# Kernel tuning notes

Measured on AMD Instinct MI355X. Metric: run time of the kernel, lower is better.

Reference implementation:

```python
import jax, jax.numpy as jnp
import numpy as np

D_MODEL = 1024
NHEAD = 16
D_K = 64
D_V = 64
B, S = 4, 2048
LN_EPS = 1e-5


def setup_inputs() -> dict:
    key = jax.random.key(0)
    ks = jax.random.split(key, 8)
    inv = 1.0 / np.sqrt(D_MODEL)
    return {
        "Q_input": jax.random.normal(ks[0], (B, S, D_MODEL), jnp.float32),
        "K_input": jax.random.normal(ks[1], (B, S, D_MODEL), jnp.float32),
        "V_input": jax.random.normal(ks[2], (B, S, D_MODEL), jnp.float32),
        "attn_mask": jnp.zeros((B, S, S), dtype=bool),
        # Linear weights stored as [in, out] for x @ W
        "W_Q": jax.random.uniform(ks[3], (D_MODEL, NHEAD * D_K), jnp.float32, -inv, inv),
        "W_K": jax.random.uniform(ks[4], (D_MODEL, NHEAD * D_K), jnp.float32, -inv, inv),
        "W_V": jax.random.uniform(ks[5], (D_MODEL, NHEAD * D_V), jnp.float32, -inv, inv),
        "W_fc": jax.random.uniform(ks[6], (NHEAD * D_V, D_MODEL), jnp.float32, -inv, inv),
        "ln_gamma": jnp.ones((D_MODEL,), jnp.float32),
        "ln_beta": jnp.zeros((D_MODEL,), jnp.float32),
    }


def reference(Q_input, K_input, V_input, attn_mask, W_Q, W_K, W_V, W_fc, ln_gamma, ln_beta):
    b = Q_input.shape[0]
    # QKV projections -> [b, h, s, d]
    Q = (Q_input @ W_Q).reshape(b, -1, NHEAD, D_K).transpose(0, 2, 1, 3)
    K = (K_input @ W_K).reshape(b, -1, NHEAD, D_K).transpose(0, 2, 1, 3)
    V = (V_input @ W_V).reshape(b, -1, NHEAD, D_V).transpose(0, 2, 1, 3)
    # NOTE faithful quirk: divide by sqrt(temperature) = sqrt(sqrt(d_k)) = d_k**0.25
    scale = np.sqrt(D_K ** 0.5).astype(np.float32)
    score = jnp.einsum('bhqd,bhkd->bhqk', Q, K) / scale
    score = jnp.where(attn_mask[:, None, :, :], jnp.float32(-1e9), score)
    attn = jax.nn.softmax(score, axis=-1)
    out = jnp.einsum('bhqk,bhkd->bhqd', attn, V)  # [b,h,s,d_v]
    out = out.transpose(0, 2, 1, 3).reshape(b, -1, NHEAD * D_V)
    q = out @ W_fc + Q_input  # residual
    mu = jnp.mean(q, axis=-1, keepdims=True)
    var = jnp.mean(jnp.square(q - mu), axis=-1, keepdims=True)
    q = (q - mu) / jnp.sqrt(var + LN_EPS) * ln_gamma + ln_beta
    return (q, attn)
```

## Files before the change

### kernel.cpp

```cpp
#include <hip/hip_runtime.h>
#include <hip/hip_bf16.h>
#include <stdint.h>

#define D_MODEL 1024
#define NHEAD   16
#define DK      64
#define BB      4
#define SS      2048
#define MROWS   (BB*SS)
#define KDIM    1024

typedef __attribute__((ext_vector_type(8))) short short8;
typedef __attribute__((ext_vector_type(4))) short bf16x4;
typedef __attribute__((ext_vector_type(4))) float f32x4;

static __device__ __forceinline__ unsigned short f2bf(float f) {
    union { float f; unsigned u; } v; v.f = f;
    unsigned r = v.u + 0x7FFFu + ((v.u >> 16) & 1u);
    return (unsigned short)(r >> 16);
}
static __device__ __forceinline__ float bf2f(unsigned short s) {
    union { unsigned u; float f; } v; v.u = ((unsigned)s) << 16;
    return v.f;
}

#define LDS_RD8(base, byteoff) (*(const short8*)((const char*)(base) + (byteoff)))

__global__ __launch_bounds__(256) void k_conv(const float* __restrict__ src,
                                              unsigned short* __restrict__ dst, int n) {
    int i = (blockIdx.x * 256 + threadIdx.x) * 4;
    if (i < n) {
        float4 v = *(const float4*)(src + i);
        ushort4 o;
        o.x = f2bf(v.x); o.y = f2bf(v.y); o.z = f2bf(v.z); o.w = f2bf(v.w);
        *(ushort4*)(dst + i) = o;
    }
}

__global__ __launch_bounds__(256) void k_transpose(const float* __restrict__ W,
                                                   unsigned short* __restrict__ WT) {
    __shared__ float t[32][33];
    int bx = blockIdx.x, by = blockIdx.y;
    int tx = threadIdx.x & 31, ty = threadIdx.x >> 5;
#pragma unroll
    for (int k = 0; k < 4; k++) {
        int r = by * 32 + ty + k * 8;
        t[ty + k * 8][tx] = W[(size_t)r * 1024 + bx * 32 + tx];
    }
    __syncthreads();
#pragma unroll
    for (int k = 0; k < 4; k++) {
        int c = bx * 32 + ty + k * 8;
        WT[(size_t)c * 1024 + by * 32 + tx] = f2bf(t[tx][ty + k * 8]);
    }
}

template<int MODE>
__global__ __launch_bounds__(256) void k_gemm(const unsigned short* __restrict__ A,
                                              const unsigned short* __restrict__ BT,
                                              unsigned short* __restrict__ out,
                                              const float* __restrict__ resid) {
    __shared__ __align__(16) unsigned short As[128 * 32];
    __shared__ __align__(16) unsigned short Bs[128 * 32];
    int m0 = blockIdx.x * 128;
    int n0 = blockIdx.y * 128;
    int tid = threadIdx.x;
    int lane = tid & 63, w = tid >> 6;
    int wm = w >> 1, wn = w & 1;
    int lo = lane & 15, hi = lane >> 4;

    f32x4 acc[4][4];
#pragma unroll
    for (int i = 0; i < 4; i++)
#pragma unroll
        for (int j = 0; j < 4; j++) acc[i][j] = (f32x4){0.f, 0.f, 0.f, 0.f};

    for (int k0 = 0; k0 < KDIM; k0 += 32) {
#pragma unroll
        for (int c = 0; c < 2; c++) {
            int idx = c * 256 + tid;
            int row = idx >> 2, ko = (idx & 3) * 8;
            __builtin_amdgcn_global_load_lds(
                (const __attribute__((address_space(1))) void*)(A + (size_t)(m0 + row) * KDIM + k0 + ko),
                (__attribute__((address_space(3))) void*)((char*)As + idx * 16), 16, 0, 0);
            __builtin_amdgcn_global_load_lds(
                (const __attribute__((address_space(1))) void*)(BT + (size_t)(n0 + row) * KDIM + k0 + ko),
                (__attribute__((address_space(3))) void*)((char*)Bs + idx * 16), 16, 0, 0);
        }
        __syncthreads();
        short8 a[4], b[4];
#pragma unroll
        for (int i = 0; i < 4; i++)
            a[i] = *(const short8*)(As + (wm * 64 + i * 16 + lo) * 32 + hi * 8);
#pragma unroll
        for (int j = 0; j < 4; j++)
            b[j] = *(const short8*)(Bs + (wn * 64 + j * 16 + lo) * 32 + hi * 8);
#pragma unroll
        for (int i = 0; i < 4; i++)
#pragma unroll
            for (int j = 0; j < 4; j++)
                acc[i][j] = __builtin_amdgcn_mfma_f32_16x16x32_bf16(a[i], b[j], acc[i][j], 0, 0, 0);
        __syncthreads();
    }

#pragma unroll
    for (int i = 0; i < 4; i++)
#pragma unroll
        for (int j = 0; j < 4; j++)
#pragma unroll
            for (int r = 0; r < 4; r++) {
                int m = m0 + wm * 64 + i * 16 + hi * 4 + r;
                int n = n0 + wn * 64 + j * 16 + lo;
                float v = acc[i][j][r];
                if (MODE == 0 || MODE == 3) {
                    if (MODE == 3) v *= 0.35355339059327373f;
                    int b_ = m >> 11, s = m & 2047, h = n >> 6, d = n & 63;
                    out[(((size_t)(b_ * NHEAD + h)) * SS + s) * DK + d] = f2bf(v);
                } else if (MODE == 1) {
                    int b_ = m >> 11, s = m & 2047, h = n >> 6, d = n & 63;
                    out[(((size_t)(b_ * NHEAD + h)) * DK + d) * SS + s] = f2bf(v);
                } else {
                    v += resid[(size_t)m * D_MODEL + n];
                    out[(size_t)m * D_MODEL + n] = f2bf(v);
                }
            }
}

static __device__ __forceinline__ void stage64(const unsigned short* __restrict__ src_base,
                                               size_t row_stride_elts,
                                               unsigned short* lds, int tid) {
#pragma unroll
    for (int i = 0; i < 2; i++) {
        int idx = i * 256 + tid;
        int r = idx >> 3, c = idx & 7;
        int sc = c ^ (r & 7);
        __builtin_amdgcn_global_load_lds(
            (const __attribute__((address_space(1))) void*)(src_base + (size_t)r * row_stride_elts + sc * 8),
            (__attribute__((address_space(3))) void*)(lds + idx * 8), 16, 0, 0);
    }
}

__global__ __launch_bounds__(256) void k_attn(const unsigned short* __restrict__ Qb,
                                              const unsigned short* __restrict__ Kb,
                                              const unsigned short* __restrict__ VTb,
                                              float* __restrict__ attn_out,
                                              unsigned short* __restrict__ O) {
    __shared__ __align__(16) unsigned short Kl[2][64 * 64];
    __shared__ __align__(16) unsigned short Vl[2][64 * 64];
    __shared__ __align__(16) unsigned short Pl[4][16 * 64];

    int bid = blockIdx.x;
    int bh = (bid & 7) * 8 + ((bid >> 3) & 7);
    int qt = bid >> 6;

    int tid = threadIdx.x;
    int w = tid >> 6, lane = tid & 63;
    int lo = lane & 15, hi = lane >> 4;
    int lo7 = lo & 7;

    const unsigned short* Qh = Qb + (size_t)bh * SS * DK;
    const unsigned short* Kh = Kb + (size_t)bh * SS * DK;
    const unsigned short* Vh = VTb + (size_t)bh * DK * SS;
    int q0 = qt * 64 + w * 16;

    short8 qa0 = *(const short8*)(Qh + (size_t)(q0 + lo) * DK + hi * 8);
    short8 qa1 = *(const short8*)(Qh + (size_t)(q0 + lo) * DK + 32 + hi * 8);

    float lsum = 0.f;
    stage64(Kh, DK, Kl[0], tid);
    {
        int cur = 0;
        for (int kt = 0; kt < SS; kt += 64, cur ^= 1) {
            __syncthreads();
            if (kt + 64 < SS) stage64(Kh + (size_t)(kt + 64) * DK, DK, Kl[cur ^ 1], tid);
            const unsigned short* KB_cur = Kl[cur];
#pragma unroll
            for (int t = 0; t < 4; t++) {
                int rbyte = (t * 16 + lo) * 128;
                short8 kb0 = LDS_RD8(KB_cur, rbyte + ((hi ^ lo7) << 4));
                short8 kb1 = LDS_RD8(KB_cur, rbyte + (((hi + 4) ^ lo7) << 4));
                f32x4 cc = (f32x4){0.f, 0.f, 0.f, 0.f};
                cc = __builtin_amdgcn_mfma_f32_16x16x32_bf16(kb0, qa0, cc, 0, 0, 0);
                cc = __builtin_amdgcn_mfma_f32_16x16x32_bf16(kb1, qa1, cc, 0, 0, 0);
#pragma unroll
                for (int r = 0; r < 4; r++) lsum += __expf(cc[r]);
            }
        }
    }
    lsum += __shfl_xor(lsum, 16);
    lsum += __shfl_xor(lsum, 32);
    float invl = 1.0f / lsum;

    f32x4 oacc[4];
#pragma unroll
    for (int d = 0; d < 4; d++) oacc[d] = (f32x4){0.f, 0.f, 0.f, 0.f};

    __syncthreads();
    stage64(Kh, DK, Kl[0], tid);
    stage64(Vh, SS, Vl[0], tid);

    unsigned short* Pw = &Pl[w][0];
    float* arow = attn_out + ((size_t)bh * SS + q0 + lo) * SS;

    {
        int cur = 0;
        for (int kt = 0; kt < SS; kt += 64, cur ^= 1) {
            __syncthreads();
            if (kt + 64 < SS) {
                stage64(Kh + (size_t)(kt + 64) * DK, DK, Kl[cur ^ 1], tid);
                stage64(Vh + (kt + 64), SS, Vl[cur ^ 1], tid);
            }
            const unsigned short* KB_cur = Kl[cur];
            const unsigned short* VB_cur = Vl[cur];
#pragma unroll
            for (int t = 0; t < 4; t++) {
                int rbyte = (t * 16 + lo) * 128;
                short8 kb0 = LDS_RD8(KB_cur, rbyte + ((hi ^ lo7) << 4));
                short8 kb1 = LDS_RD8(KB_cur, rbyte + (((hi + 4) ^ lo7) << 4));
                f32x4 cc = (f32x4){0.f, 0.f, 0.f, 0.f};
                cc = __builtin_amdgcn_mfma_f32_16x16x32_bf16(kb0, qa0, cc, 0, 0, 0);
                cc = __builtin_amdgcn_mfma_f32_16x16x32_bf16(kb1, qa1, cc, 0, 0, 0);
                float p0 = __expf(cc[0]) * invl;
                float p1 = __expf(cc[1]) * invl;
                float p2 = __expf(cc[2]) * invl;
                float p3 = __expf(cc[3]) * invl;
                float4 st; st.x = p0; st.y = p1; st.z = p2; st.w = p3;
                *(float4*)(arow + kt + t * 16 + hi * 4) = st;
                bf16x4 pk;
                pk.x = (short)f2bf(p0); pk.y = (short)f2bf(p1);
                pk.z = (short)f2bf(p2); pk.w = (short)f2bf(p3);
                *(bf16x4*)((char*)Pw + lo * 128 + ((t * 32 + hi * 8) ^ (lo7 << 4))) = pk;
            }
            asm volatile("s_waitcnt lgkmcnt(0)" ::: "memory");
            __builtin_amdgcn_sched_barrier(0);
#pragma unroll
            for (int ks = 0; ks < 2; ks++) {
                short8 af = LDS_RD8(Pw, lo * 128 + (((ks * 4 + hi) ^ lo7) << 4));
#pragma unroll
                for (int db = 0; db < 4; db++) {
                    short8 vf = LDS_RD8(VB_cur, (db * 16 + lo) * 128 + (((ks * 4 + hi) ^ lo7) << 4));
                    oacc[db] = __builtin_amdgcn_mfma_f32_16x16x32_bf16(af, vf, oacc[db], 0, 0, 0);
                }
            }
        }
    }

    int b_ = bh >> 4, h = bh & 15;
#pragma unroll
    for (int db = 0; db < 4; db++)
#pragma unroll
        for (int r = 0; r < 4; r++) {
            int s = q0 + hi * 4 + r;
            O[((size_t)b_ * SS + s) * D_MODEL + h * 64 + db * 16 + lo] = f2bf(oacc[db][r]);
        }
}

__global__ __launch_bounds__(256) void k_ln(const unsigned short* __restrict__ qpre,
                                            const float* __restrict__ gamma,
                                            const float* __restrict__ beta,
                                            float* __restrict__ outq) {
    int row = blockIdx.x;
    int tid = threadIdx.x;
    int lane = tid & 63, w = tid >> 6;
    const unsigned short* rp = qpre + (size_t)row * D_MODEL;
    ushort4 v = *(const ushort4*)(rp + tid * 4);
    float x[4] = { bf2f(v.x), bf2f(v.y), bf2f(v.z), bf2f(v.w) };
    float s1 = x[0] + x[1] + x[2] + x[3];
    float s2 = x[0]*x[0] + x[1]*x[1] + x[2]*x[2] + x[3]*x[3];
#pragma unroll
    for (int mask = 1; mask < 64; mask <<= 1) {
        s1 += __shfl_xor(s1, mask);
        s2 += __shfl_xor(s2, mask);
    }
    __shared__ float r1[4], r2[4];
    if (lane == 0) { r1[w] = s1; r2[w] = s2; }
    __syncthreads();
    float t1 = r1[0] + r1[1] + r1[2] + r1[3];
    float t2 = r2[0] + r2[1] + r2[2] + r2[3];
    float mu = t1 * (1.0f / D_MODEL);
    float var = t2 * (1.0f / D_MODEL) - mu * mu;
    float rs = rsqrtf(var + 1e-5f);
    float4 g = *(const float4*)(gamma + tid * 4);
    float4 bb = *(const float4*)(beta + tid * 4);
    float4 y;
    y.x = (x[0] - mu) * rs * g.x + bb.x;
    y.y = (x[1] - mu) * rs * g.y + bb.y;
    y.z = (x[2] - mu) * rs * g.z + bb.z;
    y.w = (x[3] - mu) * rs * g.w + bb.w;
    *(float4*)(outq + (size_t)row * D_MODEL + tid * 4) = y;
}

extern "C" void kernel_launch(void* const* d_in, const int* in_sizes, int n_in,
                              void* d_out, int out_size, void* d_ws, size_t ws_size,
                              hipStream_t stream) {
    const float* Qin  = (const float*)d_in[0];
    const float* Kin  = (const float*)d_in[1];
    const float* Vin  = (const float*)d_in[2];
    const float* WQ   = (const float*)d_in[4];
    const float* WK   = (const float*)d_in[5];
    const float* WV   = (const float*)d_in[6];
    const float* WFC  = (const float*)d_in[7];
    const float* gamma = (const float*)d_in[8];
    const float* beta  = (const float*)d_in[9];

    float* outq    = (float*)d_out;
    float* outattn = outq + (size_t)MROWS * D_MODEL;

    char* ws = (char*)d_ws;
    const size_t SZ_X = (size_t)MROWS * D_MODEL * 2;
    const size_t SZ_W = (size_t)KDIM * D_MODEL * 2;
    unsigned short* XQ   = (unsigned short*)(ws);
    unsigned short* XK   = (unsigned short*)(ws + SZ_X);
    unsigned short* XV   = (unsigned short*)(ws + 2 * SZ_X);
    unsigned short* WQT  = (unsigned short*)(ws + 3 * SZ_X);
    unsigned short* WKT  = (unsigned short*)(ws + 3 * SZ_X + SZ_W);
    unsigned short* WVT  = (unsigned short*)(ws + 3 * SZ_X + 2 * SZ_W);
    unsigned short* WFCT = (unsigned short*)(ws + 3 * SZ_X + 3 * SZ_W);
    unsigned short* QB   = (unsigned short*)(ws + 3 * SZ_X + 4 * SZ_W);
    unsigned short* KB   = (unsigned short*)(ws + 4 * SZ_X + 4 * SZ_W);
    unsigned short* VTB  = (unsigned short*)(ws + 5 * SZ_X + 4 * SZ_W);

    const int NEL = MROWS * D_MODEL;
    k_conv<<<NEL / 1024, 256, 0, stream>>>(Qin, XQ, NEL);
    k_conv<<<NEL / 1024, 256, 0, stream>>>(Kin, XK, NEL);
    k_conv<<<NEL / 1024, 256, 0, stream>>>(Vin, XV, NEL);

    dim3 tg(32, 32);
    k_transpose<<<tg, 256, 0, stream>>>(WQ, WQT);
    k_transpose<<<tg, 256, 0, stream>>>(WK, WKT);
    k_transpose<<<tg, 256, 0, stream>>>(WV, WVT);
    k_transpose<<<tg, 256, 0, stream>>>(WFC, WFCT);

    dim3 gg(MROWS / 128, D_MODEL / 128);
    k_gemm<3><<<gg, 256, 0, stream>>>(XQ, WQT, QB, nullptr);
    k_gemm<0><<<gg, 256, 0, stream>>>(XK, WKT, KB, nullptr);
    k_gemm<1><<<gg, 256, 0, stream>>>(XV, WVT, VTB, nullptr);

    unsigned short* O = XQ;
    k_attn<<<BB * NHEAD * 32, 256, 0, stream>>>(QB, KB, VTB, outattn, O);

    unsigned short* QPRE = XK;
    k_gemm<2><<<gg, 256, 0, stream>>>(O, WFCT, QPRE, Qin);

    k_ln<<<MROWS, 256, 0, stream>>>(QPRE, gamma, beta, outq);
}
```

Before: 552.4 us.

## Split attention keys across warps, cache exps in registers, batch prep launches

The attention kernel is rebuilt so each 512-thread block handles 16 queries. Its 8 warps each own a 256-key slice, and K and V are read straight from global memory instead of being staged in LDS. Exponentials are computed once and kept in registers as bf16, so the second pass that recomputes QK^T is gone. Row sums and the partial outputs of the warps are combined through shared memory. The conversion, transpose and QKV GEMM launches are each merged into one batched launch with z-indexing. The costs are a larger register footprint, normalised probabilities built from bf16-rounded exps, and uncoalesced direct global loads of K and V.

```diff
diff --git a/kernel.cpp b/kernel.cpp
--- a/kernel.cpp
+++ b/kernel.cpp
@@ -26,20 +26,30 @@
 
 #define LDS_RD8(base, byteoff) (*(const short8*)((const char*)(base) + (byteoff)))
 
-__global__ __launch_bounds__(256) void k_conv(const float* __restrict__ src,
-                                              unsigned short* __restrict__ dst, int n) {
+__global__ __launch_bounds__(256) void k_conv3(const float* __restrict__ a,
+                                               const float* __restrict__ b,
+                                               const float* __restrict__ c,
+                                               unsigned short* __restrict__ oa,
+                                               unsigned short* __restrict__ ob,
+                                               unsigned short* __restrict__ oc) {
+    const float* src = (blockIdx.y == 0) ? a : (blockIdx.y == 1) ? b : c;
+    unsigned short* dst = (blockIdx.y == 0) ? oa : (blockIdx.y == 1) ? ob : oc;
     int i = (blockIdx.x * 256 + threadIdx.x) * 4;
-    if (i < n) {
-        float4 v = *(const float4*)(src + i);
-        ushort4 o;
-        o.x = f2bf(v.x); o.y = f2bf(v.y); o.z = f2bf(v.z); o.w = f2bf(v.w);
-        *(ushort4*)(dst + i) = o;
-    }
-}
-
-__global__ __launch_bounds__(256) void k_transpose(const float* __restrict__ W,
-                                                   unsigned short* __restrict__ WT) {
+    float4 v = *(const float4*)(src + i);
+    ushort4 o;
+    o.x = f2bf(v.x); o.y = f2bf(v.y); o.z = f2bf(v.z); o.w = f2bf(v.w);
+    *(ushort4*)(dst + i) = o;
+}
+
+__global__ __launch_bounds__(256) void k_transpose4(const float* __restrict__ w0,
+                                                    const float* __restrict__ w1,
+                                                    const float* __restrict__ w2,
+                                                    const float* __restrict__ w3,
+                                                    unsigned short* __restrict__ wtbase) {
     __shared__ float t[32][33];
+    int z = blockIdx.z;
+    const float* W = (z == 0) ? w0 : (z == 1) ? w1 : (z == 2) ? w2 : w3;
+    unsigned short* WT = wtbase + (size_t)z * KDIM * D_MODEL;
     int bx = blockIdx.x, by = blockIdx.y;
     int tx = threadIdx.x & 31, ty = threadIdx.x >> 5;
 #pragma unroll
@@ -55,13 +65,18 @@
     }
 }
 
-template<int MODE>
-__global__ __launch_bounds__(256) void k_gemm(const unsigned short* __restrict__ A,
-                                              const unsigned short* __restrict__ BT,
-                                              unsigned short* __restrict__ out,
-                                              const float* __restrict__ resid) {
+__global__ __launch_bounds__(256) void k_gemm_qkv(const unsigned short* __restrict__ XQ,
+                                                  const unsigned short* __restrict__ XK,
+                                                  const unsigned short* __restrict__ XV,
+                                                  const unsigned short* __restrict__ WTbase,
+                                                  unsigned short* __restrict__ QB,
+                                                  unsigned short* __restrict__ KB,
+                                                  unsigned short* __restrict__ VTB) {
     __shared__ __align__(16) unsigned short As[128 * 32];
     __shared__ __align__(16) unsigned short Bs[128 * 32];
+    int z = blockIdx.z;
+    const unsigned short* A  = (z == 0) ? XQ : (z == 1) ? XK : XV;
+    const unsigned short* BT = WTbase + (size_t)z * KDIM * D_MODEL;
     int m0 = blockIdx.x * 128;
     int n0 = blockIdx.y * 128;
     int tid = threadIdx.x;
@@ -112,42 +127,86 @@
                 int m = m0 + wm * 64 + i * 16 + hi * 4 + r;
                 int n = n0 + wn * 64 + j * 16 + lo;
                 float v = acc[i][j][r];
-                if (MODE == 0 || MODE == 3) {
-                    if (MODE == 3) v *= 0.35355339059327373f;
-                    int b_ = m >> 11, s = m & 2047, h = n >> 6, d = n & 63;
-                    out[(((size_t)(b_ * NHEAD + h)) * SS + s) * DK + d] = f2bf(v);
-                } else if (MODE == 1) {
-                    int b_ = m >> 11, s = m & 2047, h = n >> 6, d = n & 63;
-                    out[(((size_t)(b_ * NHEAD + h)) * DK + d) * SS + s] = f2bf(v);
+                int b_ = m >> 11, s = m & 2047, h = n >> 6, d = n & 63;
+                if (z == 0) {
+                    v *= 0.35355339059327373f;
+                    QB[(((size_t)(b_ * NHEAD + h)) * SS + s) * DK + d] = f2bf(v);
+                } else if (z == 1) {
+                    KB[(((size_t)(b_ * NHEAD + h)) * SS + s) * DK + d] = f2bf(v);
                 } else {
-                    v += resid[(size_t)m * D_MODEL + n];
-                    out[(size_t)m * D_MODEL + n] = f2bf(v);
+                    VTB[(((size_t)(b_ * NHEAD + h)) * DK + d) * SS + s] = f2bf(v);
                 }
             }
 }
 
-static __device__ __forceinline__ void stage64(const unsigned short* __restrict__ src_base,
-                                               size_t row_stride_elts,
-                                               unsigned short* lds, int tid) {
-#pragma unroll
-    for (int i = 0; i < 2; i++) {
-        int idx = i * 256 + tid;
-        int r = idx >> 3, c = idx & 7;
-        int sc = c ^ (r & 7);
-        __builtin_amdgcn_global_load_lds(
-            (const __attribute__((address_space(1))) void*)(src_base + (size_t)r * row_stride_elts + sc * 8),
-            (__attribute__((address_space(3))) void*)(lds + idx * 8), 16, 0, 0);
-    }
-}
-
-__global__ __launch_bounds__(256) void k_attn(const unsigned short* __restrict__ Qb,
-                                              const unsigned short* __restrict__ Kb,
-                                              const unsigned short* __restrict__ VTb,
-                                              float* __restrict__ attn_out,
-                                              unsigned short* __restrict__ O) {
-    __shared__ __align__(16) unsigned short Kl[2][64 * 64];
-    __shared__ __align__(16) unsigned short Vl[2][64 * 64];
-    __shared__ __align__(16) unsigned short Pl[4][16 * 64];
+__global__ __launch_bounds__(256) void k_gemm_fc(const unsigned short* __restrict__ A,
+                                                 const unsigned short* __restrict__ BT,
+                                                 unsigned short* __restrict__ out,
+                                                 const float* __restrict__ resid) {
+    __shared__ __align__(16) unsigned short As[128 * 32];
+    __shared__ __align__(16) unsigned short Bs[128 * 32];
+    int m0 = blockIdx.x * 128;
+    int n0 = blockIdx.y * 128;
+    int tid = threadIdx.x;
+    int lane = tid & 63, w = tid >> 6;
+    int wm = w >> 1, wn = w & 1;
+    int lo = lane & 15, hi = lane >> 4;
+
+    f32x4 acc[4][4];
+#pragma unroll
+    for (int i = 0; i < 4; i++)
+#pragma unroll
+        for (int j = 0; j < 4; j++) acc[i][j] = (f32x4){0.f, 0.f, 0.f, 0.f};
+
+    for (int k0 = 0; k0 < KDIM; k0 += 32) {
+#pragma unroll
+        for (int c = 0; c < 2; c++) {
+            int idx = c * 256 + tid;
+            int row = idx >> 2, ko = (idx & 3) * 8;
+            __builtin_amdgcn_global_load_lds(
+                (const __attribute__((address_space(1))) void*)(A + (size_t)(m0 + row) * KDIM + k0 + ko),
+                (__attribute__((address_space(3))) void*)((char*)As + idx * 16), 16, 0, 0);
+            __builtin_amdgcn_global_load_lds(
+                (const __attribute__((address_space(1))) void*)(BT + (size_t)(n0 + row) * KDIM + k0 + ko),
+                (__attribute__((address_space(3))) void*)((char*)Bs + idx * 16), 16, 0, 0);
+        }
+        __syncthreads();
+        short8 a[4], b[4];
+#pragma unroll
+        for (int i = 0; i < 4; i++)
+            a[i] = *(const short8*)(As + (wm * 64 + i * 16 + lo) * 32 + hi * 8);
+#pragma unroll
+        for (int j = 0; j < 4; j++)
+            b[j] = *(const short8*)(Bs + (wn * 64 + j * 16 + lo) * 32 + hi * 8);
+#pragma unroll
+        for (int i = 0; i < 4; i++)
+#pragma unroll
+            for (int j = 0; j < 4; j++)
+                acc[i][j] = __builtin_amdgcn_mfma_f32_16x16x32_bf16(a[i], b[j], acc[i][j], 0, 0, 0);
+        __syncthreads();
+    }
+
+#pragma unroll
+    for (int i = 0; i < 4; i++)
+#pragma unroll
+        for (int j = 0; j < 4; j++)
+#pragma unroll
+            for (int r = 0; r < 4; r++) {
+                int m = m0 + wm * 64 + i * 16 + hi * 4 + r;
+                int n = n0 + wn * 64 + j * 16 + lo;
+                float v = acc[i][j][r] + resid[(size_t)m * D_MODEL + n];
+                out[(size_t)m * D_MODEL + n] = f2bf(v);
+            }
+}
+
+__global__ __launch_bounds__(512, 4) void k_attn(const unsigned short* __restrict__ Qb,
+                                                 const unsigned short* __restrict__ Kb,
+                                                 const unsigned short* __restrict__ VTb,
+                                                 float* __restrict__ attn_out,
+                                                 unsigned short* __restrict__ O) {
+    __shared__ float Ls[8][20];
+    __shared__ __align__(16) unsigned short Pl[8][16 * 40];
+    __shared__ __align__(16) float Or[8][16][68];
 
     int bid = blockIdx.x;
     int bh = (bid & 7) * 8 + ((bid >> 3) & 7);
@@ -156,103 +215,100 @@
     int tid = threadIdx.x;
     int w = tid >> 6, lane = tid & 63;
     int lo = lane & 15, hi = lane >> 4;
-    int lo7 = lo & 7;
 
     const unsigned short* Qh = Qb + (size_t)bh * SS * DK;
     const unsigned short* Kh = Kb + (size_t)bh * SS * DK;
     const unsigned short* Vh = VTb + (size_t)bh * DK * SS;
-    int q0 = qt * 64 + w * 16;
+    int q0 = qt * 16;
+    int kbase = w * 256;
 
     short8 qa0 = *(const short8*)(Qh + (size_t)(q0 + lo) * DK + hi * 8);
     short8 qa1 = *(const short8*)(Qh + (size_t)(q0 + lo) * DK + 32 + hi * 8);
 
+    bf16x4 Ereg[16];
     float lsum = 0.f;
-    stage64(Kh, DK, Kl[0], tid);
-    {
-        int cur = 0;
-        for (int kt = 0; kt < SS; kt += 64, cur ^= 1) {
-            __syncthreads();
-            if (kt + 64 < SS) stage64(Kh + (size_t)(kt + 64) * DK, DK, Kl[cur ^ 1], tid);
-            const unsigned short* KB_cur = Kl[cur];
-#pragma unroll
-            for (int t = 0; t < 4; t++) {
-                int rbyte = (t * 16 + lo) * 128;
-                short8 kb0 = LDS_RD8(KB_cur, rbyte + ((hi ^ lo7) << 4));
-                short8 kb1 = LDS_RD8(KB_cur, rbyte + (((hi + 4) ^ lo7) << 4));
-                f32x4 cc = (f32x4){0.f, 0.f, 0.f, 0.f};
-                cc = __builtin_amdgcn_mfma_f32_16x16x32_bf16(kb0, qa0, cc, 0, 0, 0);
-                cc = __builtin_amdgcn_mfma_f32_16x16x32_bf16(kb1, qa1, cc, 0, 0, 0);
-#pragma unroll
-                for (int r = 0; r < 4; r++) lsum += __expf(cc[r]);
-            }
-        }
+#pragma unroll
+    for (int c = 0; c < 16; c++) {
+        int kk = kbase + c * 16;
+        short8 ka0 = *(const short8*)(Kh + (size_t)(kk + lo) * DK + hi * 8);
+        short8 ka1 = *(const short8*)(Kh + (size_t)(kk + lo) * DK + 32 + hi * 8);
+        f32x4 cc = (f32x4){0.f, 0.f, 0.f, 0.f};
+        cc = __builtin_amdgcn_mfma_f32_16x16x32_bf16(ka0, qa0, cc, 0, 0, 0);
+        cc = __builtin_amdgcn_mfma_f32_16x16x32_bf16(ka1, qa1, cc, 0, 0, 0);
+        float e0 = __expf(cc[0]);
+        float e1 = __expf(cc[1]);
+        float e2 = __expf(cc[2]);
+        float e3 = __expf(cc[3]);
+        lsum += (e0 + e1) + (e2 + e3);
+        bf16x4 pk;
+        pk.x = (short)f2bf(e0); pk.y = (short)f2bf(e1);
+        pk.z = (short)f2bf(e2); pk.w = (short)f2bf(e3);
+        Ereg[c] = pk;
+        if ((c & 3) == 3) __builtin_amdgcn_sched_barrier(0);
     }
     lsum += __shfl_xor(lsum, 16);
     lsum += __shfl_xor(lsum, 32);
-    float invl = 1.0f / lsum;
+    if (lane < 16) Ls[w][lo] = lsum;
+    __syncthreads();
+    float tot = 0.f;
+#pragma unroll
+    for (int j = 0; j < 8; j++) tot += Ls[j][lo];
+    float invl = 1.0f / tot;
 
     f32x4 oacc[4];
 #pragma unroll
     for (int d = 0; d < 4; d++) oacc[d] = (f32x4){0.f, 0.f, 0.f, 0.f};
 
+    unsigned short* Pw = &Pl[w][0];
+    float* arow = attn_out + ((size_t)bh * SS + q0 + lo) * SS + kbase;
+
+#pragma unroll
+    for (int s = 0; s < 8; s++) {
+#pragma unroll
+        for (int cp = 0; cp < 2; cp++) {
+            const int c = s * 2 + cp;
+            float p0 = bf2f((unsigned short)Ereg[c].x) * invl;
+            float p1 = bf2f((unsigned short)Ereg[c].y) * invl;
+            float p2 = bf2f((unsigned short)Ereg[c].z) * invl;
+            float p3 = bf2f((unsigned short)Ereg[c].w) * invl;
+            float4 st; st.x = p0; st.y = p1; st.z = p2; st.w = p3;
+            *(float4*)(arow + c * 16 + hi * 4) = st;
+            bf16x4 pk;
+            pk.x = (short)f2bf(p0); pk.y = (short)f2bf(p1);
+            pk.z = (short)f2bf(p2); pk.w = (short)f2bf(p3);
+            *(bf16x4*)((char*)Pw + lo * 80 + cp * 32 + hi * 8) = pk;
+        }
+        short8 vf0 = *(const short8*)(Vh + (size_t)(0 * 16 + lo) * SS + kbase + s * 32 + hi * 8);
+        short8 vf1 = *(const short8*)(Vh + (size_t)(1 * 16 + lo) * SS + kbase + s * 32 + hi * 8);
+        short8 vf2 = *(const short8*)(Vh + (size_t)(2 * 16 + lo) * SS + kbase + s * 32 + hi * 8);
+        short8 vf3 = *(const short8*)(Vh + (size_t)(3 * 16 + lo) * SS + kbase + s * 32 + hi * 8);
+        asm volatile("s_waitcnt lgkmcnt(0)" ::: "memory");
+        __builtin_amdgcn_sched_barrier(0);
+        short8 af = LDS_RD8(Pw, lo * 80 + hi * 16);
+        oacc[0] = __builtin_amdgcn_mfma_f32_16x16x32_bf16(af, vf0, oacc[0], 0, 0, 0);
+        oacc[1] = __builtin_amdgcn_mfma_f32_16x16x32_bf16(af, vf1, oacc[1], 0, 0, 0);
+        oacc[2] = __builtin_amdgcn_mfma_f32_16x16x32_bf16(af, vf2, oacc[2], 0, 0, 0);
+        oacc[3] = __builtin_amdgcn_mfma_f32_16x16x32_bf16(af, vf3, oacc[3], 0, 0, 0);
+    }
+
+#pragma unroll
+    for (int db = 0; db < 4; db++)
+#pragma unroll
+        for (int r = 0; r < 4; r++)
+            Or[w][hi * 4 + r][db * 16 + lo] = oacc[db][r];
     __syncthreads();
-    stage64(Kh, DK, Kl[0], tid);
-    stage64(Vh, SS, Vl[0], tid);
-
-    unsigned short* Pw = &Pl[w][0];
-    float* arow = attn_out + ((size_t)bh * SS + q0 + lo) * SS;
-
-    {
-        int cur = 0;
-        for (int kt = 0; kt < SS; kt += 64, cur ^= 1) {
-            __syncthreads();
-            if (kt + 64 < SS) {
-                stage64(Kh + (size_t)(kt + 64) * DK, DK, Kl[cur ^ 1], tid);
-                stage64(Vh + (kt + 64), SS, Vl[cur ^ 1], tid);
-            }
-            const unsigned short* KB_cur = Kl[cur];
-            const unsigned short* VB_cur = Vl[cur];
-#pragma unroll
-            for (int t = 0; t < 4; t++) {
-                int rbyte = (t * 16 + lo) * 128;
-                short8 kb0 = LDS_RD8(KB_cur, rbyte + ((hi ^ lo7) << 4));
-                short8 kb1 = LDS_RD8(KB_cur, rbyte + (((hi + 4) ^ lo7) << 4));
-                f32x4 cc = (f32x4){0.f, 0.f, 0.f, 0.f};
-                cc = __builtin_amdgcn_mfma_f32_16x16x32_bf16(kb0, qa0, cc, 0, 0, 0);
-                cc = __builtin_amdgcn_mfma_f32_16x16x32_bf16(kb1, qa1, cc, 0, 0, 0);
-                float p0 = __expf(cc[0]) * invl;
-                float p1 = __expf(cc[1]) * invl;
-                float p2 = __expf(cc[2]) * invl;
-                float p3 = __expf(cc[3]) * invl;
-                float4 st; st.x = p0; st.y = p1; st.z = p2; st.w = p3;
-                *(float4*)(arow + kt + t * 16 + hi * 4) = st;
-                bf16x4 pk;
-                pk.x = (short)f2bf(p0); pk.y = (short)f2bf(p1);
-                pk.z = (short)f2bf(p2); pk.w = (short)f2bf(p3);
-                *(bf16x4*)((char*)Pw + lo * 128 + ((t * 32 + hi * 8) ^ (lo7 << 4))) = pk;
-            }
-            asm volatile("s_waitcnt lgkmcnt(0)" ::: "memory");
-            __builtin_amdgcn_sched_barrier(0);
-#pragma unroll
-            for (int ks = 0; ks < 2; ks++) {
-                short8 af = LDS_RD8(Pw, lo * 128 + (((ks * 4 + hi) ^ lo7) << 4));
-#pragma unroll
-                for (int db = 0; db < 4; db++) {
-                    short8 vf = LDS_RD8(VB_cur, (db * 16 + lo) * 128 + (((ks * 4 + hi) ^ lo7) << 4));
-                    oacc[db] = __builtin_amdgcn_mfma_f32_16x16x32_bf16(af, vf, oacc[db], 0, 0, 0);
-                }
-            }
-        }
-    }
-
+
+    int q = tid >> 5;
+    int d0 = (tid & 31) * 2;
+    float s0 = 0.f, s1 = 0.f;
+#pragma unroll
+    for (int j = 0; j < 8; j++) {
+        float2 v = *(const float2*)&Or[j][q][d0];
+        s0 += v.x; s1 += v.y;
+    }
     int b_ = bh >> 4, h = bh & 15;
-#pragma unroll
-    for (int db = 0; db < 4; db++)
-#pragma unroll
-        for (int r = 0; r < 4; r++) {
-            int s = q0 + hi * 4 + r;
-            O[((size_t)b_ * SS + s) * D_MODEL + h * 64 + db * 16 + lo] = f2bf(oacc[db][r]);
-        }
+    ushort2 ov; ov.x = f2bf(s0); ov.y = f2bf(s1);
+    *(ushort2*)(O + ((size_t)b_ * SS + q0 + q) * D_MODEL + h * 64 + d0) = ov;
 }
 
 __global__ __launch_bounds__(256) void k_ln(const unsigned short* __restrict__ qpre,
@@ -312,35 +368,28 @@
     unsigned short* XQ   = (unsigned short*)(ws);
     unsigned short* XK   = (unsigned short*)(ws + SZ_X);
     unsigned short* XV   = (unsigned short*)(ws + 2 * SZ_X);
-    unsigned short* WQT  = (unsigned short*)(ws + 3 * SZ_X);
-    unsigned short* WKT  = (unsigned short*)(ws + 3 * SZ_X + SZ_W);
-    unsigned short* WVT  = (unsigned short*)(ws + 3 * SZ_X + 2 * SZ_W);
+    unsigned short* WTb  = (unsigned short*)(ws + 3 * SZ_X);
     unsigned short* WFCT = (unsigned short*)(ws + 3 * SZ_X + 3 * SZ_W);
     unsigned short* QB   = (unsigned short*)(ws + 3 * SZ_X + 4 * SZ_W);
     unsigned short* KB   = (unsigned short*)(ws + 4 * SZ_X + 4 * SZ_W);
     unsigned short* VTB  = (unsigned short*)(ws + 5 * SZ_X + 4 * SZ_W);
 
     const int NEL = MROWS * D_MODEL;
-    k_conv<<<NEL / 1024, 256, 0, stream>>>(Qin, XQ, NEL);
-    k_conv<<<NEL / 1024, 256, 0, stream>>>(Kin, XK, NEL);
-    k_conv<<<NEL / 1024, 256, 0, stream>>>(Vin, XV, NEL);
-
-    dim3 tg(32, 32);
-    k_transpose<<<tg, 256, 0, stream>>>(WQ, WQT);
-    k_transpose<<<tg, 256, 0, stream>>>(WK, WKT);
-    k_transpose<<<tg, 256, 0, stream>>>(WV, WVT);
-    k_transpose<<<tg, 256, 0, stream>>>(WFC, WFCT);
-
+    dim3 cg(NEL / 1024, 3);
+    k_conv3<<<cg, 256, 0, stream>>>(Qin, Kin, Vin, XQ, XK, XV);
+
+    dim3 tg(32, 32, 4);
+    k_transpose4<<<tg, 256, 0, stream>>>(WQ, WK, WV, WFC, WTb);
+
+    dim3 gq(MROWS / 128, D_MODEL / 128, 3);
+    k_gemm_qkv<<<gq, 256, 0, stream>>>(XQ, XK, XV, WTb, QB, KB, VTB);
+
+    unsigned short* O = XQ;
+    k_attn<<<BB * NHEAD * 128, 512, 0, stream>>>(QB, KB, VTB, outattn, O);
+
+    unsigned short* QPRE = XK;
     dim3 gg(MROWS / 128, D_MODEL / 128);
-    k_gemm<3><<<gg, 256, 0, stream>>>(XQ, WQT, QB, nullptr);
-    k_gemm<0><<<gg, 256, 0, stream>>>(XK, WKT, KB, nullptr);
-    k_gemm<1><<<gg, 256, 0, stream>>>(XV, WVT, VTB, nullptr);
-
-    unsigned short* O = XQ;
-    k_attn<<<BB * NHEAD * 32, 256, 0, stream>>>(QB, KB, VTB, outattn, O);
-
-    unsigned short* QPRE = XK;
-    k_gemm<2><<<gg, 256, 0, stream>>>(O, WFCT, QPRE, Qin);
+    k_gemm_fc<<<gg, 256, 0, stream>>>(O, WFCT, QPRE, Qin);
 
     k_ln<<<MROWS, 256, 0, stream>>>(QPRE, gamma, beta, outq);
 }
```

New measurement: 706.5 us. 1.28x slower.
